# Optimization experiments

Hardware: AMD Instinct MI355X
Metric: run time of the kernel (lower is better)

Reference implementation:

```python
import jax, jax.numpy as jnp
import numpy as np

D = 1024
S = 2048
B = 4


def setup_inputs() -> dict:
    key = jax.random.key(0)
    ks = jax.random.split(key, 9)
    sc = 1.0 / np.sqrt(D)
    return {
        "x": jax.random.normal(ks[0], (B, S, D), dtype=jnp.float32),
        "Wq": jax.random.normal(ks[1], (D, D), dtype=jnp.float32) * sc,
        "bq": jax.random.normal(ks[2], (D,), dtype=jnp.float32) * 0.02,
        "Wk": jax.random.normal(ks[3], (D, D), dtype=jnp.float32) * sc,
        "bk": jax.random.normal(ks[4], (D,), dtype=jnp.float32) * 0.02,
        "Wv": jax.random.normal(ks[5], (D, D), dtype=jnp.float32) * sc,
        "bv": jax.random.normal(ks[6], (D,), dtype=jnp.float32) * 0.02,
        "Wp": jax.random.normal(ks[7], (D, D), dtype=jnp.float32) * sc,
        "bp": jax.random.normal(ks[8], (D,), dtype=jnp.float32) * 0.02,
    }


def reference(x, Wq, bq, Wk, bk, Wv, bv, Wp, bp):
    # torch nn.Linear: y = x @ W.T + b  (W stored [out, in])
    q = jnp.einsum("bsd,ed->bse", x, Wq) + bq  # [B,S,D]
    k = jnp.einsum("bsd,ed->bse", x, Wk) + bk
    v = jnp.einsum("bsd,ed->bse", x, Wv) + bv

    scale = 1.0 / jnp.sqrt(jnp.asarray(q.shape[-1], q.dtype))
    # single-head attention: contract over full embd_dim (no head split in source)
    scores = jnp.einsum("bqd,bkd->bqk", q, k) * scale  # [B,S,S]

    seq = x.shape[1]
    causal = jnp.tril(jnp.ones((seq, seq), dtype=bool))  # [S,S]
    scores = jnp.where(causal[None, :, :], scores, -jnp.inf)

    attn = jax.nn.softmax(scores, axis=-1)  # [B,S,S]
    out = jnp.einsum("bqk,bkd->bqd", attn, v)  # [B,S,D]
    out = jnp.einsum("bsd,ed->bse", out, Wp) + bp
    return out
```

## Files before the change

kernel.cpp:

```cpp
#include <hip/hip_runtime.h>

#define AS1(p) ((const __attribute__((address_space(1))) void*)(p))
#define AS3(p) ((__attribute__((address_space(3))) void*)(p))

typedef unsigned short u16;
typedef __bf16 bf16x8 __attribute__((ext_vector_type(8)));
typedef short s16x8 __attribute__((ext_vector_type(8)));
typedef float f32x4 __attribute__((ext_vector_type(4)));
typedef unsigned short u16x4 __attribute__((ext_vector_type(4)));
typedef unsigned short u16x8v __attribute__((ext_vector_type(8)));

__device__ __forceinline__ u16 f2bf(float x) {
    unsigned u = __float_as_uint(x);
    unsigned r = (u + 0x7FFFu + ((u >> 16) & 1u)) >> 16;
    return (u16)r;
}

template <typename V8>
__device__ __forceinline__ auto mfma_sel(V8 a, V8 b, f32x4 c, int)
    -> decltype(__builtin_amdgcn_mfma_f32_16x16x32_bf16(a, b, c, 0, 0, 0))
{
    return __builtin_amdgcn_mfma_f32_16x16x32_bf16(a, b, c, 0, 0, 0);
}
template <typename V8>
__device__ __forceinline__ f32x4 mfma_sel(V8 a, V8 b, f32x4 c, long)
{
    s16x8 a2 = __builtin_bit_cast(s16x8, a);
    s16x8 b2 = __builtin_bit_cast(s16x8, b);
    return __builtin_amdgcn_mfma_f32_16x16x32_bf16(a2, b2, c, 0, 0, 0);
}
__device__ __forceinline__ f32x4 mfma16x16x32(bf16x8 a, bf16x8 b, f32x4 c)
{
    return mfma_sel(a, b, c, 0);
}

__global__ __launch_bounds__(256) void cvt_bf16_kernel(const float* __restrict__ in,
                                                       u16* __restrict__ out, int n4)
{
    int i = blockIdx.x * 256 + threadIdx.x;
    if (i >= n4) return;
    float4 f = ((const float4*)in)[i];
    u16x4 o;
    o.x = f2bf(f.x); o.y = f2bf(f.y); o.z = f2bf(f.z); o.w = f2bf(f.w);
    ((u16x4*)out)[i] = o;
}

__global__ __launch_bounds__(256) void transpose16(const u16* __restrict__ in,
                                                   u16* __restrict__ out, int R, int C)
{
    __shared__ u16 tl[64][65];
    const int tr0 = blockIdx.y * 64, tc0 = blockIdx.x * 64;
    const int t = threadIdx.x;
    const int r = t >> 2, c4 = (t & 3) << 4;

    const u16* src = in + (size_t)(tr0 + r) * C + tc0 + c4;
    u16x8v a0 = *(const u16x8v*)src;
    u16x8v a1 = *(const u16x8v*)(src + 8);
    #pragma unroll
    for (int j = 0; j < 8; ++j) { tl[r][c4 + j] = a0[j]; tl[r][c4 + 8 + j] = a1[j]; }
    __syncthreads();

    u16x8v b0, b1;
    #pragma unroll
    for (int j = 0; j < 8; ++j) { b0[j] = tl[c4 + j][r]; b1[j] = tl[c4 + 8 + j][r]; }
    u16* dst = out + (size_t)(tc0 + r) * R + tr0 + c4;
    *(u16x8v*)dst = b0;
    *(u16x8v*)(dst + 8) = b1;
}

#define GBM 128
#define GBN 256
#define GBK 64
#define ABUF 16384
#define BBUF 32768
#define TBUF (ABUF + BBUF)
#define LDS_BYTES (3 * TBUF)

template <int BIAS, int OUTBF16, int CSKIP, int CKB>
__global__ __launch_bounds__(512, 2)
void gemm_nt2(const u16* __restrict__ A, const u16* __restrict__ B,
              void* __restrict__ Cv, const float* __restrict__ bias,
              void* __restrict__ C2, const float* __restrict__ bias2,
              void* __restrict__ C3, const float* __restrict__ bias3,
              int M, int N, int K, int lda, int ldb, int ldc,
              long long sA, long long sB, long long sC, float scale)
{
    extern __shared__ char smem[];

    int by = blockIdx.y;
    if (CKB) by = gridDim.y - 1 - by;
    const int m0 = by * GBM;
    const int n0 = blockIdx.x * GBN;
    if (CSKIP && n0 > m0 + GBM - 1) return;

    const int z = blockIdx.z;
    A += (size_t)z * (size_t)sA;
    B += (size_t)z * (size_t)sB;

    const int t = threadIdx.x;
    const int lane = t & 63;
    const int w = t >> 6;
    const int wr = w >> 2;
    const int wc = w & 3;
    const int fr = lane & 15, fg = lane >> 4;

    int Keff = K;
    if (CKB) { Keff = m0 + GBM; if (Keff > K) Keff = K; }
    const int nk = Keff / GBK;

    f32x4 acc[4][4] = {};

    auto STAGE = [&](int kt, int buf) {
        const int k0 = kt * GBK;
        char* sb = smem + buf * TBUF;
        #pragma unroll
        for (int i = 0; i < 2; ++i) {
            int c = t + i * 512;
            int row = c >> 3;
            int sl = (c & 7) ^ (row & 7);
            __builtin_amdgcn_global_load_lds(
                AS1(A + (size_t)(m0 + row) * lda + k0 + sl * 8),
                AS3(sb + c * 16), 16, 0, 0);
        }
        #pragma unroll
        for (int i = 0; i < 4; ++i) {
            int c = t + i * 512;
            int row = c >> 3;
            int sl = (c & 7) ^ (row & 7);
            __builtin_amdgcn_global_load_lds(
                AS1(B + (size_t)(n0 + row) * ldb + k0 + sl * 8),
                AS3(sb + ABUF + c * 16), 16, 0, 0);
        }
    };

    STAGE(0, 0);
    STAGE(1, 1);
    asm volatile("s_waitcnt vmcnt(6)" ::: "memory");
    __builtin_amdgcn_s_barrier();

    int cur = 0;
    for (int kt = 0; kt < nk; ++kt) {
        int pb = cur + 2; if (pb >= 3) pb -= 3;
        const bool pf = (kt + 2 < nk);
        if (pf) STAGE(kt + 2, pb);

        const char* la = smem + cur * TBUF;
        const char* lb = la + ABUF;
        #pragma unroll
        for (int kk = 0; kk < GBK; kk += 32) {
            const int cs = (kk >> 3) + fg;
            bf16x8 af[4], bfv[4];
            #pragma unroll
            for (int mi = 0; mi < 4; ++mi) {
                int row = wr * 64 + mi * 16 + fr;
                af[mi] = *(const bf16x8*)(la + (row << 7) + ((cs ^ (row & 7)) << 4));
            }
            #pragma unroll
            for (int ni = 0; ni < 4; ++ni) {
                int row = wc * 64 + ni * 16 + fr;
                bfv[ni] = *(const bf16x8*)(lb + (row << 7) + ((cs ^ (row & 7)) << 4));
            }
            __builtin_amdgcn_s_setprio(1);
            #pragma unroll
            for (int mi = 0; mi < 4; ++mi)
                #pragma unroll
                for (int ni = 0; ni < 4; ++ni)
                    acc[mi][ni] = mfma16x16x32(af[mi], bfv[ni], acc[mi][ni]);
            __builtin_amdgcn_s_setprio(0);
        }

        if (pf) asm volatile("s_waitcnt vmcnt(6)" ::: "memory");
        else    asm volatile("s_waitcnt vmcnt(0)" ::: "memory");
        __builtin_amdgcn_s_barrier();
        ++cur; if (cur >= 3) cur = 0;
    }

    #pragma unroll
    for (int mi = 0; mi < 4; ++mi) {
        #pragma unroll
        for (int ni = 0; ni < 4; ++ni) {
            int col = n0 + wc * 64 + ni * 16 + fr;
            u16* dst16 = (u16*)Cv;
            float* dst32 = (float*)Cv;
            float bval = 0.f, sc_ = scale;
            int ccol = col;
            if (BIAS == 1) bval = bias[col];
            if (BIAS == 3) {
                int seg = col >> 10; ccol = col & 1023;
                if (seg == 0)      { dst16 = (u16*)Cv; bval = bias[ccol]; }
                else if (seg == 1) { dst16 = (u16*)C2; bval = bias2[ccol]; sc_ = 1.f; }
                else               { dst16 = (u16*)C3; bval = bias3[ccol]; sc_ = 1.f; }
            }
            #pragma unroll
            for (int j = 0; j < 4; ++j) {
                int row = m0 + wr * 64 + mi * 16 + fg * 4 + j;
                float v = (acc[mi][ni][j] + bval) * sc_;
                size_t off = (size_t)z * (size_t)sC + (size_t)row * ldc + ccol;
                if (OUTBF16 || BIAS == 3) dst16[off] = f2bf(v);
                else                      dst32[off] = v;
            }
        }
    }
}

__device__ __forceinline__ float waveMax(float v) {
    #pragma unroll
    for (int o = 32; o > 0; o >>= 1) v = fmaxf(v, __shfl_xor(v, o));
    return v;
}
__device__ __forceinline__ float waveSum(float v) {
    #pragma unroll
    for (int o = 32; o > 0; o >>= 1) v += __shfl_xor(v, o);
    return v;
}

__global__ __launch_bounds__(256) void softmax_causal_kernel(float* __restrict__ scores, int S)
{
    __shared__ float red[4];
    const int gb = blockIdx.x;
    const int b = gb / S;
    const int i = gb - b * S;
    float* srow = scores + (size_t)b * S * S + (size_t)i * S;
    u16* prow = (u16*)srow;
    const int t = threadIdx.x;
    const int jlim = ((i >> 7) + 1) << 7;

    float vals[8];
    float mx = -1e30f;
    #pragma unroll
    for (int s = 0; s < 8; ++s) {
        int j = t + (s << 8);
        float x = -1e30f;
        if (j <= i) x = srow[j];
        vals[s] = x;
        mx = fmaxf(mx, x);
    }
    mx = waveMax(mx);
    const int wv = t >> 6;
    if ((t & 63) == 0) red[wv] = mx;
    __syncthreads();
    mx = fmaxf(fmaxf(red[0], red[1]), fmaxf(red[2], red[3]));
    __syncthreads();

    float sum = 0.f;
    #pragma unroll
    for (int s = 0; s < 8; ++s) {
        float e = (vals[s] > -1e29f) ? __expf(vals[s] - mx) : 0.f;
        vals[s] = e;
        sum += e;
    }
    sum = waveSum(sum);
    if ((t & 63) == 0) red[wv] = sum;
    __syncthreads();
    sum = red[0] + red[1] + red[2] + red[3];
    const float inv = 1.f / sum;
    __syncthreads();

    #pragma unroll
    for (int s = 0; s < 8; ++s) {
        int j = t + (s << 8);
        if (j < jlim) prow[j] = f2bf(vals[s] * inv);
    }
}

extern "C" void kernel_launch(void* const* d_in, const int* in_sizes, int n_in,
                              void* d_out, int out_size, void* d_ws, size_t ws_size,
                              hipStream_t stream)
{
    (void)in_sizes; (void)n_in; (void)out_size;
    const float* x  = (const float*)d_in[0];
    const float* Wq = (const float*)d_in[1];
    const float* bq = (const float*)d_in[2];
    const float* Wk = (const float*)d_in[3];
    const float* bk = (const float*)d_in[4];
    const float* Wv = (const float*)d_in[5];
    const float* bv = (const float*)d_in[6];
    const float* Wp = (const float*)d_in[7];
    const float* bp = (const float*)d_in[8];

    const int D = 1024, S = 2048, B = 4;
    const int M = B * S;

    char* p = (char*)d_ws;
    u16* xb   = (u16*)p; p += (size_t)M * D * 2;
    u16* Wcat = (u16*)p; p += (size_t)3 * D * D * 2;
    u16* Wpb  = (u16*)p; p += (size_t)D * D * 2;
    u16* qb   = (u16*)p; p += (size_t)M * D * 2;
    u16* kb   = (u16*)p; p += (size_t)M * D * 2;
    u16* vTb  = (u16*)p; p += (size_t)M * D * 2;
    u16* vb   = (u16*)p;
    float* sc = (float*)p;
    u16* attnb = xb;

    const size_t fixed = (size_t)p - (size_t)d_ws;
    const size_t sb1   = (size_t)S * S * 4;
    int zb = (ws_size >= fixed + 4 * sb1) ? 4 : 1;

    hipFuncSetAttribute((const void*)gemm_nt2<3, 1, 0, 0>,
                        hipFuncAttributeMaxDynamicSharedMemorySize, LDS_BYTES);
    hipFuncSetAttribute((const void*)gemm_nt2<0, 0, 1, 0>,
                        hipFuncAttributeMaxDynamicSharedMemorySize, LDS_BYTES);
    hipFuncSetAttribute((const void*)gemm_nt2<0, 1, 0, 1>,
                        hipFuncAttributeMaxDynamicSharedMemorySize, LDS_BYTES);
    hipFuncSetAttribute((const void*)gemm_nt2<1, 0, 0, 0>,
                        hipFuncAttributeMaxDynamicSharedMemorySize, LDS_BYTES);

    cvt_bf16_kernel<<<(M * D / 4 + 255) / 256, 256, 0, stream>>>(x, xb, M * D / 4);
    cvt_bf16_kernel<<<(D * D / 4 + 255) / 256, 256, 0, stream>>>(Wq, Wcat, D * D / 4);
    cvt_bf16_kernel<<<(D * D / 4 + 255) / 256, 256, 0, stream>>>(Wk, Wcat + (size_t)D * D, D * D / 4);
    cvt_bf16_kernel<<<(D * D / 4 + 255) / 256, 256, 0, stream>>>(Wv, Wcat + (size_t)2 * D * D, D * D / 4);
    cvt_bf16_kernel<<<(D * D / 4 + 255) / 256, 256, 0, stream>>>(Wp, Wpb, D * D / 4);

    gemm_nt2<3, 1, 0, 0><<<dim3(3 * D / GBN, M / GBM, 1), 512, LDS_BYTES, stream>>>(
        xb, Wcat, qb, bq, kb, bk, vb, bv,
        M, 3 * D, D, D, D, D, 0, 0, 0, 0.03125f);

    transpose16<<<dim3(D / 64, M / 64), 256, 0, stream>>>(vb, vTb, M, D);

    for (int b0 = 0; b0 < B; b0 += zb) {
        gemm_nt2<0, 0, 1, 0><<<dim3(S / GBN, S / GBM, zb), 512, LDS_BYTES, stream>>>(
            qb + (size_t)b0 * S * D, kb + (size_t)b0 * S * D, sc, nullptr,
            nullptr, nullptr, nullptr, nullptr,
            S, S, D, D, D, S,
            (long long)S * D, (long long)S * D, (long long)S * S, 1.0f);
        softmax_causal_kernel<<<zb * S, 256, 0, stream>>>(sc, S);
        gemm_nt2<0, 1, 0, 1><<<dim3(D / GBN, S / GBM, zb), 512, LDS_BYTES, stream>>>(
            (const u16*)sc, vTb + (size_t)b0 * S, attnb + (size_t)b0 * S * D, nullptr,
            nullptr, nullptr, nullptr, nullptr,
            S, D, S, 2 * S, M, D,
            (long long)2 * S * S, (long long)S, (long long)S * D, 1.0f);
    }

    gemm_nt2<1, 0, 0, 0><<<dim3(D / GBN, M / GBM, 1), 512, LDS_BYTES, stream>>>(
        attnb, Wpb, d_out, bp, nullptr, nullptr, nullptr, nullptr,
        M, D, D, D, D, D, 0, 0, 0, 1.0f);
}
```

Measured before the change: 210.3 us.

## Template GEMM on N tile width and split prefetch across K sub-steps

Makes the GEMM tile width a template parameter, so the score, attention-times-V and output projection GEMMs use 128-wide N tiles (twice the blocks, smaller LDS), while the QKV projection keeps 256. The prefetch of the next stage is split into two phases interleaved with the two 32-wide K sub-steps, with barriers around each MFMA block, to spread global loads and improve overlap and occupancy. It also adds extra barriers per K step and lowers per-block data reuse on the narrower tiles.

```diff
diff --git a/kernel.cpp b/kernel.cpp
--- a/kernel.cpp
+++ b/kernel.cpp
@@ -69,14 +69,9 @@
 }
 
 #define GBM 128
-#define GBN 256
 #define GBK 64
-#define ABUF 16384
-#define BBUF 32768
-#define TBUF (ABUF + BBUF)
-#define LDS_BYTES (3 * TBUF)
-
-template <int BIAS, int OUTBF16, int CSKIP, int CKB>
+
+template <int TN, int BIAS, int OUTBF16, int CSKIP, int CKB>
 __global__ __launch_bounds__(512, 2)
 void gemm_nt2(const u16* __restrict__ A, const u16* __restrict__ B,
               void* __restrict__ Cv, const float* __restrict__ bias,
@@ -85,12 +80,17 @@
               int M, int N, int K, int lda, int ldb, int ldc,
               long long sA, long long sB, long long sC, float scale)
 {
+    constexpr int BN    = TN * 64;
+    constexpr int ABUF_ = GBM * GBK * 2;
+    constexpr int BBUF_ = BN * GBK * 2;
+    constexpr int TBUF_ = ABUF_ + BBUF_;
+    constexpr int BL    = TN;
     extern __shared__ char smem[];
 
     int by = blockIdx.y;
     if (CKB) by = gridDim.y - 1 - by;
     const int m0 = by * GBM;
-    const int n0 = blockIdx.x * GBN;
+    const int n0 = blockIdx.x * BN;
     if (CSKIP && n0 > m0 + GBM - 1) return;
 
     const int z = blockIdx.z;
@@ -108,78 +108,90 @@
     if (CKB) { Keff = m0 + GBM; if (Keff > K) Keff = K; }
     const int nk = Keff / GBK;
 
-    f32x4 acc[4][4] = {};
-
-    auto STAGE = [&](int kt, int buf) {
+    f32x4 acc[4][TN] = {};
+
+    auto STAGE = [&](int kt, int buf, int ph) {
         const int k0 = kt * GBK;
-        char* sb = smem + buf * TBUF;
+        char* sb = smem + buf * TBUF_;
+        if (ph == 0) {
+            #pragma unroll
+            for (int i = 0; i < 2; ++i) {
+                int c = t + i * 512;
+                int row = c >> 3;
+                int sl = (c & 7) ^ (row & 7);
+                __builtin_amdgcn_global_load_lds(
+                    AS1(A + (size_t)(m0 + row) * lda + k0 + sl * 8),
+                    AS3(sb + c * 16), 16, 0, 0);
+            }
+        }
+        const int ib = ph ? BL / 2 : 0;
+        const int ie = ph ? BL : BL / 2;
         #pragma unroll
-        for (int i = 0; i < 2; ++i) {
-            int c = t + i * 512;
-            int row = c >> 3;
-            int sl = (c & 7) ^ (row & 7);
-            __builtin_amdgcn_global_load_lds(
-                AS1(A + (size_t)(m0 + row) * lda + k0 + sl * 8),
-                AS3(sb + c * 16), 16, 0, 0);
-        }
-        #pragma unroll
-        for (int i = 0; i < 4; ++i) {
+        for (int i = ib; i < ie; ++i) {
             int c = t + i * 512;
             int row = c >> 3;
             int sl = (c & 7) ^ (row & 7);
             __builtin_amdgcn_global_load_lds(
                 AS1(B + (size_t)(n0 + row) * ldb + k0 + sl * 8),
-                AS3(sb + ABUF + c * 16), 16, 0, 0);
+                AS3(sb + ABUF_ + c * 16), 16, 0, 0);
         }
     };
 
-    STAGE(0, 0);
-    STAGE(1, 1);
-    asm volatile("s_waitcnt vmcnt(6)" ::: "memory");
+    STAGE(0, 0, 0); STAGE(0, 0, 1);
+    STAGE(1, 1, 0); STAGE(1, 1, 1);
+    if (TN == 4) asm volatile("s_waitcnt vmcnt(6)" ::: "memory");
+    else         asm volatile("s_waitcnt vmcnt(4)" ::: "memory");
     __builtin_amdgcn_s_barrier();
 
     int cur = 0;
     for (int kt = 0; kt < nk; ++kt) {
         int pb = cur + 2; if (pb >= 3) pb -= 3;
         const bool pf = (kt + 2 < nk);
-        if (pf) STAGE(kt + 2, pb);
-
-        const char* la = smem + cur * TBUF;
-        const char* lb = la + ABUF;
+        const char* la = smem + cur * TBUF_;
+        const char* lb = la + ABUF_;
+
         #pragma unroll
         for (int kk = 0; kk < GBK; kk += 32) {
+            const int ph = kk >> 5;
             const int cs = (kk >> 3) + fg;
-            bf16x8 af[4], bfv[4];
+            bf16x8 af[4], bfv[TN];
             #pragma unroll
             for (int mi = 0; mi < 4; ++mi) {
                 int row = wr * 64 + mi * 16 + fr;
                 af[mi] = *(const bf16x8*)(la + (row << 7) + ((cs ^ (row & 7)) << 4));
             }
             #pragma unroll
-            for (int ni = 0; ni < 4; ++ni) {
-                int row = wc * 64 + ni * 16 + fr;
+            for (int ni = 0; ni < TN; ++ni) {
+                int row = wc * (TN * 16) + ni * 16 + fr;
                 bfv[ni] = *(const bf16x8*)(lb + (row << 7) + ((cs ^ (row & 7)) << 4));
             }
+            if (pf) STAGE(kt + 2, pb, ph);
+            if (ph == 1) {
+                if (pf) {
+                    if (TN == 4) asm volatile("s_waitcnt vmcnt(6)" ::: "memory");
+                    else         asm volatile("s_waitcnt vmcnt(4)" ::: "memory");
+                } else {
+                    asm volatile("s_waitcnt vmcnt(0)" ::: "memory");
+                }
+            }
+            __builtin_amdgcn_s_barrier();
             __builtin_amdgcn_s_setprio(1);
             #pragma unroll
             for (int mi = 0; mi < 4; ++mi)
                 #pragma unroll
-                for (int ni = 0; ni < 4; ++ni)
+                for (int ni = 0; ni < TN; ++ni)
                     acc[mi][ni] = mfma16x16x32(af[mi], bfv[ni], acc[mi][ni]);
             __builtin_amdgcn_s_setprio(0);
+            __builtin_amdgcn_s_barrier();
         }
-
-        if (pf) asm volatile("s_waitcnt vmcnt(6)" ::: "memory");
-        else    asm volatile("s_waitcnt vmcnt(0)" ::: "memory");
-        __builtin_amdgcn_s_barrier();
         ++cur; if (cur >= 3) cur = 0;
     }
 
     #pragma unroll
     for (int mi = 0; mi < 4; ++mi) {
         #pragma unroll
-        for (int ni = 0; ni < 4; ++ni) {
-            int col = n0 + wc * 64 + ni * 16 + fr;
+        for (int ni = 0; ni < TN; ++ni) {
+            int col = n0 + wc * (TN * 16) + ni * 16 + fr;
             u16* dst16 = (u16*)Cv;
             float* dst32 = (float*)Cv;
             float bval = 0.f, sc_ = scale;
@@ -296,14 +308,17 @@
     const size_t sb1   = (size_t)S * S * 4;
     int zb = (ws_size >= fixed + 4 * sb1) ? 4 : 1;
 
-    hipFuncSetAttribute((const void*)gemm_nt2<3, 1, 0, 0>,
-                        hipFuncAttributeMaxDynamicSharedMemorySize, LDS_BYTES);
-    hipFuncSetAttribute((const void*)gemm_nt2<0, 0, 1, 0>,
-                        hipFuncAttributeMaxDynamicSharedMemorySize, LDS_BYTES);
-    hipFuncSetAttribute((const void*)gemm_nt2<0, 1, 0, 1>,
-                        hipFuncAttributeMaxDynamicSharedMemorySize, LDS_BYTES);
-    hipFuncSetAttribute((const void*)gemm_nt2<1, 0, 0, 0>,
-                        hipFuncAttributeMaxDynamicSharedMemorySize, LDS_BYTES);
+    const int LDS4 = 3 * (16384 + 32768);
+    const int LDS2 = 3 * (16384 + 16384);
+
+    hipFuncSetAttribute((const void*)gemm_nt2<4, 3, 1, 0, 0>,
+                        hipFuncAttributeMaxDynamicSharedMemorySize, LDS4);
+    hipFuncSetAttribute((const void*)gemm_nt2<2, 0, 0, 1, 0>,
+                        hipFuncAttributeMaxDynamicSharedMemorySize, LDS2);
+    hipFuncSetAttribute((const void*)gemm_nt2<2, 0, 1, 0, 1>,
+                        hipFuncAttributeMaxDynamicSharedMemorySize, LDS2);
+    hipFuncSetAttribute((const void*)gemm_nt2<2, 1, 0, 0, 0>,
+                        hipFuncAttributeMaxDynamicSharedMemorySize, LDS2);
 
     cvt_bf16_kernel<<<(M * D / 4 + 255) / 256, 256, 0, stream>>>(x, xb, M * D / 4);
     cvt_bf16_kernel<<<(D * D / 4 + 255) / 256, 256, 0, stream>>>(Wq, Wcat, D * D / 4);
@@ -311,27 +326,27 @@
     cvt_bf16_kernel<<<(D * D / 4 + 255) / 256, 256, 0, stream>>>(Wv, Wcat + (size_t)2 * D * D, D * D / 4);
     cvt_bf16_kernel<<<(D * D / 4 + 255) / 256, 256, 0, stream>>>(Wp, Wpb, D * D / 4);
 
-    gemm_nt2<3, 1, 0, 0><<<dim3(3 * D / GBN, M / GBM, 1), 512, LDS_BYTES, stream>>>(
+    gemm_nt2<4, 3, 1, 0, 0><<<dim3(3 * D / 256, M / GBM, 1), 512, LDS4, stream>>>(
         xb, Wcat, qb, bq, kb, bk, vb, bv,
         M, 3 * D, D, D, D, D, 0, 0, 0, 0.03125f);
 
     transpose16<<<dim3(D / 64, M / 64), 256, 0, stream>>>(vb, vTb, M, D);
 
     for (int b0 = 0; b0 < B; b0 += zb) {
-        gemm_nt2<0, 0, 1, 0><<<dim3(S / GBN, S / GBM, zb), 512, LDS_BYTES, stream>>>(
+        gemm_nt2<2, 0, 0, 1, 0><<<dim3(S / 128, S / GBM, zb), 512, LDS2, stream>>>(
             qb + (size_t)b0 * S * D, kb + (size_t)b0 * S * D, sc, nullptr,
             nullptr, nullptr, nullptr, nullptr,
             S, S, D, D, D, S,
             (long long)S * D, (long long)S * D, (long long)S * S, 1.0f);
         softmax_causal_kernel<<<zb * S, 256, 0, stream>>>(sc, S);
-        gemm_nt2<0, 1, 0, 1><<<dim3(D / GBN, S / GBM, zb), 512, LDS_BYTES, stream>>>(
+        gemm_nt2<2, 0, 1, 0, 1><<<dim3(D / 128, S / GBM, zb), 512, LDS2, stream>>>(
             (const u16*)sc, vTb + (size_t)b0 * S, attnb + (size_t)b0 * S * D, nullptr,
             nullptr, nullptr, nullptr, nullptr,
             S, D, S, 2 * S, M, D,
             (long long)2 * S * S, (long long)S, (long long)S * D, 1.0f);
     }
 
-    gemm_nt2<1, 0, 0, 0><<<dim3(D / GBN, M / GBM, 1), 512, LDS_BYTES, stream>>>(
+    gemm_nt2<2, 1, 0, 0, 0><<<dim3(D / 128, M / GBM, 1), 512, LDS2, stream>>>(
         attnb, Wpb, d_out, bp, nullptr, nullptr, nullptr, nullptr,
         M, D, D, D, D, D, 0, 0, 0, 1.0f);
 }
```

After: 231.4 us. 1.1x slower.

## Add dedicated 256x256 QKV GEMM writing transposed V, merge weight conversions

Applied to the files above, without the earlier changes.

Replaces the generic QKV projection GEMM with a dedicated 256x256-tile kernel (BK=32, triple-buffered LDS, XCD-aware block remapping) whose epilogue writes Q (pre-scaled), K, and V already transposed. This removes the separate transpose kernel and the intermediate V buffer. It also merges four weight-conversion launches into one 2D-grid kernel. The larger tile raises register pressure (8x4 accumulators per wave) and the transposed V store is a strided 8-byte write per fragment.

```diff
diff --git a/kernel.cpp b/kernel.cpp
--- a/kernel.cpp
+++ b/kernel.cpp
@@ -8,7 +8,6 @@
 typedef short s16x8 __attribute__((ext_vector_type(8)));
 typedef float f32x4 __attribute__((ext_vector_type(4)));
 typedef unsigned short u16x4 __attribute__((ext_vector_type(4)));
-typedef unsigned short u16x8v __attribute__((ext_vector_type(8)));
 
 __device__ __forceinline__ u16 f2bf(float x) {
     unsigned u = __float_as_uint(x);
@@ -45,27 +44,22 @@
     ((u16x4*)out)[i] = o;
 }
 
-__global__ __launch_bounds__(256) void transpose16(const u16* __restrict__ in,
-                                                   u16* __restrict__ out, int R, int C)
-{
-    __shared__ u16 tl[64][65];
-    const int tr0 = blockIdx.y * 64, tc0 = blockIdx.x * 64;
-    const int t = threadIdx.x;
-    const int r = t >> 2, c4 = (t & 3) << 4;
-
-    const u16* src = in + (size_t)(tr0 + r) * C + tc0 + c4;
-    u16x8v a0 = *(const u16x8v*)src;
-    u16x8v a1 = *(const u16x8v*)(src + 8);
-    #pragma unroll
-    for (int j = 0; j < 8; ++j) { tl[r][c4 + j] = a0[j]; tl[r][c4 + 8 + j] = a1[j]; }
-    __syncthreads();
-
-    u16x8v b0, b1;
-    #pragma unroll
-    for (int j = 0; j < 8; ++j) { b0[j] = tl[c4 + j][r]; b1[j] = tl[c4 + 8 + j][r]; }
-    u16* dst = out + (size_t)(tc0 + r) * R + tr0 + c4;
-    *(u16x8v*)dst = b0;
-    *(u16x8v*)(dst + 8) = b1;
+__global__ __launch_bounds__(256) void cvt_w4_kernel(const float* __restrict__ Wq,
+                                                     const float* __restrict__ Wk,
+                                                     const float* __restrict__ Wv,
+                                                     const float* __restrict__ Wp,
+                                                     u16* __restrict__ Wcat,
+                                                     u16* __restrict__ Wpb, int n4)
+{
+    int i = blockIdx.x * 256 + threadIdx.x;
+    if (i >= n4) return;
+    const int by = blockIdx.y;
+    const float* src = (by == 0) ? Wq : (by == 1) ? Wk : (by == 2) ? Wv : Wp;
+    u16* dst = (by == 3) ? Wpb : (Wcat + (size_t)by * n4 * 4);
+    float4 f = ((const float4*)src)[i];
+    u16x4 o;
+    o.x = f2bf(f.x); o.y = f2bf(f.y); o.z = f2bf(f.z); o.w = f2bf(f.w);
+    ((u16x4*)dst)[i] = o;
 }
 
 #define GBM 128
@@ -74,14 +68,12 @@
 #define ABUF 16384
 #define BBUF 32768
 #define TBUF (ABUF + BBUF)
-#define LDS_BYTES (3 * TBUF)
+#define LDS_NT2 (3 * TBUF)
 
 template <int BIAS, int OUTBF16, int CSKIP, int CKB>
 __global__ __launch_bounds__(512, 2)
 void gemm_nt2(const u16* __restrict__ A, const u16* __restrict__ B,
               void* __restrict__ Cv, const float* __restrict__ bias,
-              void* __restrict__ C2, const float* __restrict__ bias2,
-              void* __restrict__ C3, const float* __restrict__ bias3,
               int M, int N, int K, int lda, int ldb, int ldc,
               long long sA, long long sB, long long sC, float scale)
 {
@@ -180,24 +172,139 @@
         #pragma unroll
         for (int ni = 0; ni < 4; ++ni) {
             int col = n0 + wc * 64 + ni * 16 + fr;
-            u16* dst16 = (u16*)Cv;
-            float* dst32 = (float*)Cv;
-            float bval = 0.f, sc_ = scale;
-            int ccol = col;
-            if (BIAS == 1) bval = bias[col];
-            if (BIAS == 3) {
-                int seg = col >> 10; ccol = col & 1023;
-                if (seg == 0)      { dst16 = (u16*)Cv; bval = bias[ccol]; }
-                else if (seg == 1) { dst16 = (u16*)C2; bval = bias2[ccol]; sc_ = 1.f; }
-                else               { dst16 = (u16*)C3; bval = bias3[ccol]; sc_ = 1.f; }
-            }
+            float bval = (BIAS == 1) ? bias[col] : 0.f;
             #pragma unroll
             for (int j = 0; j < 4; ++j) {
                 int row = m0 + wr * 64 + mi * 16 + fg * 4 + j;
-                float v = (acc[mi][ni][j] + bval) * sc_;
-                size_t off = (size_t)z * (size_t)sC + (size_t)row * ldc + ccol;
-                if (OUTBF16 || BIAS == 3) dst16[off] = f2bf(v);
-                else                      dst32[off] = v;
+                float v = (acc[mi][ni][j] + bval) * scale;
+                size_t off = (size_t)z * (size_t)sC + (size_t)row * ldc + col;
+                if (OUTBF16) ((u16*)Cv)[off] = f2bf(v);
+                else         ((float*)Cv)[off] = v;
+            }
+        }
+    }
+}
+
+#define QBM 256
+#define QBK 32
+#define QABUF 16384
+#define QTBUF 32768
+#define QLDS  98304
+
+__global__ __launch_bounds__(512, 2)
+void gemm256_qkv(const u16* __restrict__ A, const u16* __restrict__ B,
+                 u16* __restrict__ q, const float* __restrict__ bq,
+                 u16* __restrict__ ko, const float* __restrict__ bk,
+                 u16* __restrict__ vT, const float* __restrict__ bv,
+                 int M, int K, float qscale)
+{
+    extern __shared__ char smem[];
+
+    const int gx = gridDim.x;
+    const int nwg = gx * gridDim.y;
+    int id = blockIdx.y * gx + blockIdx.x;
+    id = (id & 7) * (nwg >> 3) + (id >> 3);
+    const int bx = id % gx;
+    const int by = id / gx;
+    const int m0 = by * QBM;
+    const int n0 = bx * 256;
+
+    const int t = threadIdx.x;
+    const int lane = t & 63;
+    const int w = t >> 6;
+    const int wr = w >> 2;
+    const int wc = w & 3;
+    const int fr = lane & 15, fg = lane >> 4;
+
+    const int nk = K / QBK;
+
+    f32x4 acc[8][4] = {};
+
+    auto STAGE = [&](int kt, int buf) {
+        const int k0 = kt * QBK;
+        char* sb = smem + buf * QTBUF;
+        #pragma unroll
+        for (int i = 0; i < 2; ++i) {
+            int c = t + i * 512;
+            int row = c >> 2;
+            int sl = (c & 3) ^ ((row >> 1) & 3);
+            __builtin_amdgcn_global_load_lds(
+                AS1(A + (size_t)(m0 + row) * K + k0 + sl * 8),
+                AS3(sb + c * 16), 16, 0, 0);
+        }
+        #pragma unroll
+        for (int i = 0; i < 2; ++i) {
+            int c = t + i * 512;
+            int row = c >> 2;
+            int sl = (c & 3) ^ ((row >> 1) & 3);
+            __builtin_amdgcn_global_load_lds(
+                AS1(B + (size_t)(n0 + row) * K + k0 + sl * 8),
+                AS3(sb + QABUF + c * 16), 16, 0, 0);
+        }
+    };
+
+    STAGE(0, 0);
+    STAGE(1, 1);
+    asm volatile("s_waitcnt vmcnt(4)" ::: "memory");
+    __builtin_amdgcn_s_barrier();
+
+    int cur = 0;
+    for (int kt = 0; kt < nk; ++kt) {
+        int pb = cur + 2; if (pb >= 3) pb -= 3;
+        const bool pf = (kt + 2 < nk);
+        if (pf) STAGE(kt + 2, pb);
+
+        const char* la = smem + cur * QTBUF;
+        const char* lb = la + QABUF;
+        bf16x8 af[8], bfv[4];
+        #pragma unroll
+        for (int mi = 0; mi < 8; ++mi) {
+            int row = wr * 128 + mi * 16 + fr;
+            af[mi] = *(const bf16x8*)(la + (row << 6) + ((fg ^ ((row >> 1) & 3)) << 4));
+        }
+        #pragma unroll
+        for (int ni = 0; ni < 4; ++ni) {
+            int row = wc * 64 + ni * 16 + fr;
+            bfv[ni] = *(const bf16x8*)(lb + (row << 6) + ((fg ^ ((row >> 1) & 3)) << 4));
+        }
+        __builtin_amdgcn_s_setprio(1);
+        #pragma unroll
+        for (int mi = 0; mi < 8; ++mi)
+            #pragma unroll
+            for (int ni = 0; ni < 4; ++ni)
+                acc[mi][ni] = mfma16x16x32(af[mi], bfv[ni], acc[mi][ni]);
+        __builtin_amdgcn_s_setprio(0);
+
+        if (pf) asm volatile("s_waitcnt vmcnt(4)" ::: "memory");
+        else    asm volatile("s_waitcnt vmcnt(0)" ::: "memory");
+        __builtin_amdgcn_s_barrier();
+        ++cur; if (cur >= 3) cur = 0;
+    }
+
+    const int seg = n0 >> 10;
+    #pragma unroll
+    for (int mi = 0; mi < 8; ++mi) {
+        #pragma unroll
+        for (int ni = 0; ni < 4; ++ni) {
+            int col = n0 + wc * 64 + ni * 16 + fr;
+            int ccol = col & 1023;
+            int row0 = m0 + wr * 128 + mi * 16 + fg * 4;
+            if (seg == 0) {
+                float b = bq[ccol];
+                #pragma unroll
+                for (int j = 0; j < 4; ++j)
+                    q[(size_t)(row0 + j) * 1024 + ccol] = f2bf((acc[mi][ni][j] + b) * qscale);
+            } else if (seg == 1) {
+                float b = bk[ccol];
+                #pragma unroll
+                for (int j = 0; j < 4; ++j)
+                    ko[(size_t)(row0 + j) * 1024 + ccol] = f2bf(acc[mi][ni][j] + b);
+            } else {
+                float b = bv[ccol];
+                u16x4 o;
+                #pragma unroll
+                for (int j = 0; j < 4; ++j) o[j] = f2bf(acc[mi][ni][j] + b);
+                *(u16x4*)&vT[(size_t)ccol * M + row0] = o;
             }
         }
     }
@@ -288,7 +395,6 @@
     u16* qb   = (u16*)p; p += (size_t)M * D * 2;
     u16* kb   = (u16*)p; p += (size_t)M * D * 2;
     u16* vTb  = (u16*)p; p += (size_t)M * D * 2;
-    u16* vb   = (u16*)p;
     float* sc = (float*)p;
     u16* attnb = xb;
 
@@ -296,42 +402,35 @@
     const size_t sb1   = (size_t)S * S * 4;
     int zb = (ws_size >= fixed + 4 * sb1) ? 4 : 1;
 
-    hipFuncSetAttribute((const void*)gemm_nt2<3, 1, 0, 0>,
-                        hipFuncAttributeMaxDynamicSharedMemorySize, LDS_BYTES);
+    hipFuncSetAttribute((const void*)gemm256_qkv,
+                        hipFuncAttributeMaxDynamicSharedMemorySize, QLDS);
     hipFuncSetAttribute((const void*)gemm_nt2<0, 0, 1, 0>,
-                        hipFuncAttributeMaxDynamicSharedMemorySize, LDS_BYTES);
+                        hipFuncAttributeMaxDynamicSharedMemorySize, LDS_NT2);
     hipFuncSetAttribute((const void*)gemm_nt2<0, 1, 0, 1>,
-                        hipFuncAttributeMaxDynamicSharedMemorySize, LDS_BYTES);
+                        hipFuncAttributeMaxDynamicSharedMemorySize, LDS_NT2);
     hipFuncSetAttribute((const void*)gemm_nt2<1, 0, 0, 0>,
-                        hipFuncAttributeMaxDynamicSharedMemorySize, LDS_BYTES);
+                        hipFuncAttributeMaxDynamicSharedMemorySize, LDS_NT2);
 
     cvt_bf16_kernel<<<(M * D / 4 + 255) / 256, 256, 0, stream>>>(x, xb, M * D / 4);
-    cvt_bf16_kernel<<<(D * D / 4 + 255) / 256, 256, 0, stream>>>(Wq, Wcat, D * D / 4);
-    cvt_bf16_kernel<<<(D * D / 4 + 255) / 256, 256, 0, stream>>>(Wk, Wcat + (size_t)D * D, D * D / 4);
-    cvt_bf16_kernel<<<(D * D / 4 + 255) / 256, 256, 0, stream>>>(Wv, Wcat + (size_t)2 * D * D, D * D / 4);
-    cvt_bf16_kernel<<<(D * D / 4 + 255) / 256, 256, 0, stream>>>(Wp, Wpb, D * D / 4);
-
-    gemm_nt2<3, 1, 0, 0><<<dim3(3 * D / GBN, M / GBM, 1), 512, LDS_BYTES, stream>>>(
-        xb, Wcat, qb, bq, kb, bk, vb, bv,
-        M, 3 * D, D, D, D, D, 0, 0, 0, 0.03125f);
-
-    transpose16<<<dim3(D / 64, M / 64), 256, 0, stream>>>(vb, vTb, M, D);
+    cvt_w4_kernel<<<dim3((D * D / 4 + 255) / 256, 4), 256, 0, stream>>>(
+        Wq, Wk, Wv, Wp, Wcat, Wpb, D * D / 4);
+
+    gemm256_qkv<<<dim3(3 * D / 256, M / QBM), 512, QLDS, stream>>>(
+        xb, Wcat, qb, bq, kb, bk, vTb, bv, M, D, 0.03125f);
 
     for (int b0 = 0; b0 < B; b0 += zb) {
-        gemm_nt2<0, 0, 1, 0><<<dim3(S / GBN, S / GBM, zb), 512, LDS_BYTES, stream>>>(
+        gemm_nt2<0, 0, 1, 0><<<dim3(S / GBN, S / GBM, zb), 512, LDS_NT2, stream>>>(
             qb + (size_t)b0 * S * D, kb + (size_t)b0 * S * D, sc, nullptr,
-            nullptr, nullptr, nullptr, nullptr,
             S, S, D, D, D, S,
             (long long)S * D, (long long)S * D, (long long)S * S, 1.0f);
         softmax_causal_kernel<<<zb * S, 256, 0, stream>>>(sc, S);
-        gemm_nt2<0, 1, 0, 1><<<dim3(D / GBN, S / GBM, zb), 512, LDS_BYTES, stream>>>(
+        gemm_nt2<0, 1, 0, 1><<<dim3(D / GBN, S / GBM, zb), 512, LDS_NT2, stream>>>(
             (const u16*)sc, vTb + (size_t)b0 * S, attnb + (size_t)b0 * S * D, nullptr,
-            nullptr, nullptr, nullptr, nullptr,
             S, D, S, 2 * S, M, D,
             (long long)2 * S * S, (long long)S, (long long)S * D, 1.0f);
     }
 
-    gemm_nt2<1, 0, 0, 0><<<dim3(D / GBN, M / GBM, 1), 512, LDS_BYTES, stream>>>(
-        attnb, Wpb, d_out, bp, nullptr, nullptr, nullptr, nullptr,
+    gemm_nt2<1, 0, 0, 0><<<dim3(D / GBN, M / GBM, 1), 512, LDS_NT2, stream>>>(
+        attnb, Wpb, d_out, bp,
         M, D, D, D, D, D, 0, 0, 0, 1.0f);
 }
```

New measurement: 205.3 us. 1.02x faster.
